# Kernel optimization log

Measured on AMD Instinct MI355X. Metric: run time of the kernel, lower is better.

Reference implementation:

```python
import jax, jax.numpy as jnp
import numpy as np

# ---- db4 filters (pywt conventions: dec_lo = rec_lo[::-1], rec_hi = qmf(rec_lo)) ----
F = 8  # db4 filter length
_rec_lo = np.array([0.23037781330885523, 0.7148465705525415, 0.6308807679295904,
                    -0.027983769416983849, -0.18703481171888114, 0.030841381835986965,
                    0.032883011666982945, -0.010597401784997278], dtype=np.float32)
_rec_hi = _rec_lo[::-1].copy()
_rec_hi[1::2] *= -1.0
REC_LO = jnp.asarray(_rec_lo)
REC_HI = jnp.asarray(_rec_hi)

MAX_LEVEL = 9  # pywt.dwt_max_level(4096, 8)


def _conv1d(x, kernel, stride=1, padding='VALID', lhs_dilation=None):
    # x: [B, L] -> correlation (XLA conv does NOT flip the kernel)
    out = jax.lax.conv_general_dilated(
        x[:, None, :], kernel[None, None, :],
        window_strides=(stride,), padding=padding,
        lhs_dilation=lhs_dilation,
        dimension_numbers=('NCH', 'OIH', 'NCH'))
    return out[:, 0, :]


def dwt(x):
    # pywt.dwt(x, 'db4', mode='symmetric'):
    # cA = np.convolve(sym_ext(x, F-1), dec_lo, 'valid')[1::2]
    # convolution with dec filter == correlation with rec filter (its reverse)
    ext = jnp.pad(x, ((0, 0), (F - 1, F - 1)), mode='symmetric')[:, 1:]
    return _conv1d(ext, REC_LO, stride=2), _conv1d(ext, REC_HI, stride=2)


def idwt(ca, cd):
    # pywt.idwt: zero-upsample coeffs, full convolution with rec filters, trim edges
    n = ca.shape[1]
    pad = ((F - 1, F - 1),)
    out = (_conv1d(ca, REC_LO[::-1], padding=pad, lhs_dilation=(2,)) +
           _conv1d(cd, REC_HI[::-1], padding=pad, lhs_dilation=(2,)))
    return out[:, F - 2:2 * n]  # output length = 2n - F + 2


def wavelet_features(x1):
    # Faithful to WaveletDWTLayer stack + WaveletParsingLayer: at each level k>=2,
    # reconstruct with details of levels k and k-1 only (others zeroed), with
    # pywt.waverec's trim-by-one rule; concatenate the 8 full-length reconstructions.
    a = x1
    cds, recs = [], []
    for level in range(1, MAX_LEVEL + 1):
        a, d = dwt(a)
        if level >= 2:
            r = idwt(jnp.zeros_like(d), d)
            for j in range(level - 2, -1, -1):
                dj = cds[j] if j == level - 2 else jnp.zeros_like(cds[j])
                if r.shape[1] == dj.shape[1] + 1:  # waverec trim rule
                    r = r[:, :-1]
                r = idwt(r, dj)
            recs.append(r)  # [B, signal_length]
        cds.append(d)
    return jnp.concatenate(recs, axis=1)  # [B, signal_length*(MAX_LEVEL-1)]


def reference(x1, x2, x3, W0, b0, W1, b1, W2, b2):
    # x2/x3 are placeholders in the original module (overwritten by layers 1/2)
    h = wavelet_features(x1)
    for W, b in ((W0, b0), (W1, b1), (W2, b2)):
        h = jax.nn.relu(h) @ W.T + b
    return h


def setup_inputs() -> dict:
    key = jax.random.key(0)
    ks = jax.random.split(key, 4)
    B, N = 2048, 4096
    D_IN, H1, H2, OUT = 32768, 181, 13, 10
    return {
        'x1': jax.random.normal(ks[0], (B, N), jnp.float32),
        'x2': jnp.zeros((B, 1, 8), jnp.float32),
        'x3': jnp.zeros((B, 1, 8), jnp.float32),
        'W0': jax.random.normal(ks[1], (H1, D_IN), jnp.float32) / np.float32(np.sqrt(D_IN)),
        'b0': jnp.zeros((H1,), jnp.float32),
        'W1': jax.random.normal(ks[2], (H2, H1), jnp.float32) / np.float32(np.sqrt(H1)),
        'b1': jnp.zeros((H2,), jnp.float32),
        'W2': jax.random.normal(ks[3], (OUT, H2), jnp.float32) / np.float32(np.sqrt(H2)),
        'b2': jnp.zeros((OUT,), jnp.float32),
    }
```

## Files before the change

kernel.cpp:

```cpp
#include <hip/hip_runtime.h>
#include <hip/hip_bf16.h>


typedef _Float16 f16x8 __attribute__((ext_vector_type(8)));
typedef _Float16 f16x4v __attribute__((ext_vector_type(4)));
typedef float f32x4 __attribute__((ext_vector_type(4)));

#define WV_THREADS 256
#define DROW 4160
#define NSPLIT 32
#define KCHUNK 1024
#define GEMM_BM 256

#define L0 0.23037781330885523f
#define L1 0.7148465705525415f
#define L2f 0.6308807679295904f
#define L3 -0.02798376941698385f
#define L4 -0.18703481171888114f
#define L5 0.030841381835986965f
#define L6 0.032883011666982945f
#define L7 -0.010597401784997278f

#define H0 -0.010597401784997278f
#define H1 -0.032883011666982945f
#define H2 0.030841381835986965f
#define H3 0.18703481171888114f
#define H4 -0.02798376941698385f
#define H5 -0.6308807679295904f
#define H6 0.7148465705525415f
#define H7 -0.23037781330885523f

__constant__ constexpr int cNL[10]   = {4096, 2051, 1029, 518, 262, 134, 70, 38, 22, 14};
__constant__ constexpr int cDOFF[10] = {0, 0, 2052, 3084, 3604, 3868, 4004, 4076, 4116, 4140};

__device__ __forceinline__ int ext_idx(int j, int n) {
  return (j < 6) ? (5 - j) : ((j < n + 6) ? (j - 6) : (2 * n + 5 - j));
}

__device__ __forceinline__ void dwt2(const float* a, float* anext, float* d,
                                     int n, int m, bool store_a) {
  const int ng = (m + 1) >> 1;
  for (int g = threadIdx.x; g < ng; g += WV_THREADS) {
    float w[10];
    if (g >= 2 && 4 * g + 9 <= n + 5) {
      const float2* af = (const float2*)a + (2 * g - 3);
      float2 b0 = af[0], b1 = af[1], b2 = af[2], b3 = af[3], b4 = af[4];
      w[0] = b0.x; w[1] = b0.y; w[2] = b1.x; w[3] = b1.y; w[4] = b2.x;
      w[5] = b2.y; w[6] = b3.x; w[7] = b3.y; w[8] = b4.x; w[9] = b4.y;
    } else {
#pragma unroll
      for (int q = 0; q < 10; ++q) {
        int j = 4 * g + q;
        int jm = n + 12;
        if (j > jm) j = jm;
        w[q] = a[ext_idx(j, n)];
      }
    }
    float sl0 = w[0]*L0 + w[1]*L1 + w[2]*L2f + w[3]*L3 + w[4]*L4 + w[5]*L5 + w[6]*L6 + w[7]*L7;
    float sh0 = w[0]*H0 + w[1]*H1 + w[2]*H2  + w[3]*H3 + w[4]*H4 + w[5]*H5 + w[6]*H6 + w[7]*H7;
    float sl1 = w[2]*L0 + w[3]*L1 + w[4]*L2f + w[5]*L3 + w[6]*L4 + w[7]*L5 + w[8]*L6 + w[9]*L7;
    float sh1 = w[2]*H0 + w[3]*H1 + w[4]*H2  + w[5]*H3 + w[6]*H4 + w[7]*H5 + w[8]*H6 + w[9]*H7;
    if (2 * g + 1 < m) {
      if (store_a) *(float2*)(anext + 2 * g) = make_float2(sl0, sl1);
      *(float2*)(d + 2 * g) = make_float2(sh0, sh1);
    } else {
      if (store_a) anext[2 * g] = sl0;
      d[2 * g] = sh0;
    }
  }
}

#define SWZ(u) ((u) ^ (((u) >> 3) & 7))
__device__ __forceinline__ const float4* lds4c(const float* b, int s) {
  return (const float4*)b + SWZ(s);
}
__device__ __forceinline__ float4* lds4(float* b, int s) {
  return (float4*)b + SWZ(s);
}

template <int NP>
__device__ __forceinline__ void lvlL(const float* a, float* v) {
#pragma unroll
  for (int q = 0; q < NP; ++q) {
    v[2*q]   = a[q+3]*L0 + a[q+2]*L2f + a[q+1]*L4 + a[q]*L6;
    v[2*q+1] = a[q+3]*L1 + a[q+2]*L3  + a[q+1]*L5 + a[q]*L7;
  }
}
template <int NP>
__device__ __forceinline__ void lvlH(const float* d, float* v) {
#pragma unroll
  for (int q = 0; q < NP; ++q) {
    v[2*q]   = d[q+3]*H0 + d[q+2]*H2 + d[q+1]*H4 + d[q]*H6;
    v[2*q+1] = d[q+3]*H1 + d[q+2]*H3 + d[q+1]*H5 + d[q]*H7;
  }
}
template <int NP>
__device__ __forceinline__ void lvlLH(const float* a, const float* d, float* v) {
#pragma unroll
  for (int q = 0; q < NP; ++q) {
    v[2*q]   = a[q+3]*L0 + a[q+2]*L2f + a[q+1]*L4 + a[q]*L6
             + d[q+3]*H0 + d[q+2]*H2  + d[q+1]*H4 + d[q]*H6;
    v[2*q+1] = a[q+3]*L1 + a[q+2]*L3  + a[q+1]*L5 + a[q]*L7
             + d[q+3]*H1 + d[q+2]*H3  + d[q+1]*H5 + d[q]*H7;
  }
}

__device__ __forceinline__ void g8f2(const float* p, int s, float* w) {
#pragma unroll
  for (int i = 0; i < 4; ++i) {
    float2 v = *(const float2*)(p + s + 2 * i);
    w[2*i] = v.x; w[2*i+1] = v.y;
  }
}
__device__ __forceinline__ void g12f4(const float* p, int s, float* w) {
#pragma unroll
  for (int i = 0; i < 3; ++i) {
    float4 v = *(const float4*)(p + s + 4 * i);
    w[4*i] = v.x; w[4*i+1] = v.y; w[4*i+2] = v.z; w[4*i+3] = v.w;
  }
}

__device__ __forceinline__ void store16(_Float16* outg, int t, const float* v) {
  f16x8 h0, h1;
#pragma unroll
  for (int i = 0; i < 8; ++i) h0[i] = (_Float16)fmaxf(v[i], 0.f);
#pragma unroll
  for (int i = 0; i < 8; ++i) h1[i] = (_Float16)fmaxf(v[8 + i], 0.f);
  *(f16x8*)(outg + 16 * t) = h0;
  *(f16x8*)(outg + 16 * t + 8) = h1;
}

__device__ __forceinline__ void fin2(const float* d2, const float* d1, _Float16* og) {
  const int t = threadIdx.x;
  float dw[12];  g12f4(d2, 4 * t, dw);
  float mid[12]; lvlH<6>(dw, mid);
  float d1w[12]; g12f4(d1, 8 * t, d1w);
  float v[16];   lvlLH<8>(mid, d1w, v);
  store16(og, t, v);
}

__device__ __forceinline__ void fin3(const float* d3, const float* d2, _Float16* og) {
  const int t = threadIdx.x;
  float dw[8];   g8f2(d3, 2 * t, dw);
  float v0[10];  lvlH<5>(dw, v0);
  float d2w[12]; g12f4(d2, 4 * t, d2w);
  float v1[12];  lvlLH<6>(v0, d2w, v1);
  float v[16];   lvlL<8>(v1, v);
  store16(og, t, v);
}

__device__ __forceinline__ void fin4(const float* d4, const float* d3, _Float16* og) {
  const int t = threadIdx.x;
  float dw[7];
#pragma unroll
  for (int i = 0; i < 7; ++i) dw[i] = d4[t + i];
  float v0[8];   lvlH<4>(dw, v0);
  float d3w[8];  g8f2(d3, 2 * t, d3w);
  float v1[10];  lvlLH<5>(v0, d3w, v1);
  float v2[12];  lvlL<6>(v1, v2);
  float v[16];   lvlL<8>(v2, v);
  store16(og, t, v);
}

template <bool HAS_CA, bool HAS_CD, bool FINAL, int N>
__device__ __forceinline__ void step16(const float* ca, const float* cd,
                                       float* outl, _Float16* outg) {
  constexpr int npair = N - 3;
  constexpr int ng = (npair + 7) >> 3;
  const int t = threadIdx.x;
  if (t >= ng) return;
  float w[12], v[12];
  if constexpr (HAS_CA) {
    float4 a = *lds4c(ca, 2 * t), b = *lds4c(ca, 2 * t + 1), c = *lds4c(ca, 2 * t + 2);
    w[0]=a.x; w[1]=a.y; w[2]=a.z; w[3]=a.w; w[4]=b.x; w[5]=b.y; w[6]=b.z; w[7]=b.w;
    w[8]=c.x; w[9]=c.y; w[10]=c.z; w[11]=c.w;
  }
  if constexpr (HAS_CD) {
    const float4* p = (const float4*)(cd + 8 * t);
    float4 a = p[0], b = p[1], c = p[2];
    v[0]=a.x; v[1]=a.y; v[2]=a.z; v[3]=a.w; v[4]=b.x; v[5]=b.y; v[6]=b.z; v[7]=b.w;
    v[8]=c.x; v[9]=c.y; v[10]=c.z; v[11]=c.w;
  }
  float E[8], O[8];
#pragma unroll
  for (int pp = 0; pp < 8; ++pp) {
    float e = 0.f, o = 0.f;
    if constexpr (HAS_CA) {
      e = w[pp+3]*L0 + w[pp+2]*L2f + w[pp+1]*L4 + w[pp]*L6;
      o = w[pp+3]*L1 + w[pp+2]*L3  + w[pp+1]*L5 + w[pp]*L7;
    }
    if constexpr (HAS_CD) {
      e += v[pp+3]*H0 + v[pp+2]*H2 + v[pp+1]*H4 + v[pp]*H6;
      o += v[pp+3]*H1 + v[pp+2]*H3 + v[pp+1]*H5 + v[pp]*H7;
    }
    E[pp] = e; O[pp] = o;
  }
  if constexpr (FINAL) {
    float vv[16];
#pragma unroll
    for (int q = 0; q < 8; ++q) { vv[2*q] = E[q]; vv[2*q+1] = O[q]; }
    store16(outg, t, vv);
  } else {
#pragma unroll
    for (int j = 0; j < 4; ++j) {
      const int p2 = 8 * t + 2 * j;
      if (p2 + 1 < npair) {
        *lds4(outl, 4 * t + j) = make_float4(E[2*j], O[2*j], E[2*j+1], O[2*j+1]);
      } else if (p2 < npair) {
        *(float2*)lds4(outl, 4 * t + j) = make_float2(E[2*j], O[2*j]);
      }
    }
  }
}

__device__ __forceinline__ void nocd2_core(const float w[12], float r[11],
                                           float E[8], float O[8]) {
#pragma unroll
  for (int h = 0; h < 6; ++h) {
    float e = w[h+3]*L0 + w[h+2]*L2f + w[h+1]*L4 + w[h]*L6;
    float o = w[h+3]*L1 + w[h+2]*L3  + w[h+1]*L5 + w[h]*L7;
    r[2*h] = e;
    if (2*h + 1 < 11) r[2*h+1] = o;
  }
#pragma unroll
  for (int pp = 0; pp < 8; ++pp) {
    E[pp] = r[pp+3]*L0 + r[pp+2]*L2f + r[pp+1]*L4 + r[pp]*L6;
    O[pp] = r[pp+3]*L1 + r[pp+2]*L3  + r[pp+1]*L5 + r[pp]*L7;
  }
}

template <int N1>
__device__ __forceinline__ void pair16(const float* cur, float* outl) {
  constexpr int N2 = (2 * N1 - 6 == 1030) ? 1029 : (2 * N1 - 6);
  constexpr int np2 = N2 - 3;
  constexpr int ng = (np2 + 7) >> 3;
  const int t = threadIdx.x;
  if (t >= ng) return;
  float w[12];
  float4 a = *lds4c(cur, t), b = *lds4c(cur, t + 1), c = *lds4c(cur, t + 2);
  w[0]=a.x; w[1]=a.y; w[2]=a.z; w[3]=a.w; w[4]=b.x; w[5]=b.y; w[6]=b.z; w[7]=b.w;
  w[8]=c.x; w[9]=c.y; w[10]=c.z; w[11]=c.w;
  float r[11], E[8], O[8];
  nocd2_core(w, r, E, O);
#pragma unroll
  for (int j = 0; j < 4; ++j) {
    const int p2 = 8 * t + 2 * j;
    if (p2 + 1 < np2) {
      *lds4(outl, 4 * t + j) = make_float4(E[2*j], O[2*j], E[2*j+1], O[2*j+1]);
    } else if (p2 < np2) {
      *(float2*)lds4(outl, 4 * t + j) = make_float2(E[2*j], O[2*j]);
    }
  }
}

__device__ __forceinline__ void finpair16(const float* cur, _Float16* outg) {
  const int t = threadIdx.x;
  float w[12];
  float4 a = *lds4c(cur, t), b = *lds4c(cur, t + 1), c = *lds4c(cur, t + 2);
  w[0]=a.x; w[1]=a.y; w[2]=a.z; w[3]=a.w; w[4]=b.x; w[5]=b.y; w[6]=b.z; w[7]=b.w;
  w[8]=c.x; w[9]=c.y; w[10]=c.z; w[11]=c.w;
  float r[11], E[8], O[8];
  nocd2_core(w, r, E, O);
  float vv[16];
#pragma unroll
  for (int q = 0; q < 8; ++q) { vv[2*q] = E[q]; vv[2*q+1] = O[q]; }
  store16(outg, t, vv);
}

template <int NL, int NLm1>
__device__ __forceinline__ void initpair16(const float* cdL, const float* cdm,
                                           float* outl) {
  constexpr int np2 = NLm1 - 3;
  constexpr int ng = (np2 + 7) >> 3;
  const int t = threadIdx.x;
  if (t >= ng) return;
  float w[12];
  {
    const float4* p = (const float4*)(cdL + 4 * t);
    float4 a = p[0], b = p[1], c = p[2];
    w[0]=a.x; w[1]=a.y; w[2]=a.z; w[3]=a.w; w[4]=b.x; w[5]=b.y; w[6]=b.z; w[7]=b.w;
    w[8]=c.x; w[9]=c.y; w[10]=c.z; w[11]=c.w;
  }
  float r[11];
#pragma unroll
  for (int h = 0; h < 6; ++h) {
    float e = w[h+3]*H0 + w[h+2]*H2 + w[h+1]*H4 + w[h]*H6;
    float o = w[h+3]*H1 + w[h+2]*H3 + w[h+1]*H5 + w[h]*H7;
    r[2*h] = e;
    if (2*h + 1 < 11) r[2*h+1] = o;
  }
  float v[12];
  {
    const float4* p = (const float4*)(cdm + 8 * t);
    float4 a = p[0], b = p[1], c = p[2];
    v[0]=a.x; v[1]=a.y; v[2]=a.z; v[3]=a.w; v[4]=b.x; v[5]=b.y; v[6]=b.z; v[7]=b.w;
    v[8]=c.x; v[9]=c.y; v[10]=c.z; v[11]=c.w;
  }
  float E[8], O[8];
#pragma unroll
  for (int pp = 0; pp < 8; ++pp) {
    E[pp] = r[pp+3]*L0 + r[pp+2]*L2f + r[pp+1]*L4 + r[pp]*L6
          + v[pp+3]*H0 + v[pp+2]*H2  + v[pp+1]*H4 + v[pp]*H6;
    O[pp] = r[pp+3]*L1 + r[pp+2]*L3  + r[pp+1]*L5 + r[pp]*L7
          + v[pp+3]*H1 + v[pp+2]*H3  + v[pp+1]*H5 + v[pp]*H7;
  }
#pragma unroll
  for (int j = 0; j < 4; ++j) {
    const int p2 = 8 * t + 2 * j;
    if (p2 + 1 < np2) {
      *lds4(outl, 4 * t + j) = make_float4(E[2*j], O[2*j], E[2*j+1], O[2*j+1]);
    } else if (p2 < np2) {
      *(float2*)lds4(outl, 4 * t + j) = make_float2(E[2*j], O[2*j]);
    }
  }
}

__global__ __launch_bounds__(WV_THREADS) void wv_analysis_cvt(
    const float* __restrict__ x, float* __restrict__ dG,
    const float* __restrict__ W0, _Float16* __restrict__ Bw) {
  __shared__ float r1[4104];
  __shared__ float r2[2056];
  const int tid = threadIdx.x;

  if (blockIdx.x >= 2048) {
    size_t i = ((size_t)(blockIdx.x - 2048) * 256 + tid) * 4;
    int rowc = (int)(i >> 15);
    f16x4v h;
    if (rowc < 181) {
      const float4 v = *(const float4*)(W0 + i);
      h[0] = (_Float16)v.x; h[1] = (_Float16)v.y;
      h[2] = (_Float16)v.z; h[3] = (_Float16)v.w;
    } else {
      h[0] = (_Float16)0.f; h[1] = (_Float16)0.f;
      h[2] = (_Float16)0.f; h[3] = (_Float16)0.f;
    }
    *(f16x4v*)(Bw + i) = h;
    return;
  }

  const int NLa[10]  = {4096, 2051, 1029, 518, 262, 134, 70, 38, 22, 14};
  const int DOFF[10] = {0, 0, 2052, 3084, 3604, 3868, 4004, 4076, 4116, 4140};
  const int LOFF[10] = {0, 0, 1036, 520, 2068, 1040, 2332, 1176, 2404, 1216};
  const int row = blockIdx.x;

  const float4* xr = (const float4*)(x + (size_t)row * 4096);
  for (int i = tid; i < 1024; i += WV_THREADS) ((float4*)r1)[i] = xr[i];
  __syncthreads();

  float* dr = dG + (size_t)row * DROW;
  dwt2(r1, r2, dr + DOFF[1], NLa[0], NLa[1], true);
  __syncthreads();
  const float* ap = r2;
  float* an = r1;
  for (int lev = 2; lev <= 9; ++lev) {
    float* dbuf = ((lev & 1) ? r2 : r1) + LOFF[lev];
    dwt2(ap, an, dbuf, NLa[lev - 1], NLa[lev], lev < 9);
    __syncthreads();
    const float* t = ap; ap = an; an = (float*)t;
  }
  for (int lev = 2; lev <= 9; ++lev) {
    const float* src = ((lev & 1) ? r2 : r1) + LOFF[lev];
    float* dst = dr + DOFF[lev];
    const int n = NLa[lev];
    for (int i = 2 * tid; i + 1 < n; i += 2 * WV_THREADS)
      *(float2*)(dst + i) = *(const float2*)(src + i);
    if ((n & 1) && tid == 0) dst[n - 1] = src[n - 1];
  }
}

__global__ __launch_bounds__(WV_THREADS, 8) void wv_synth(
    const float* __restrict__ dG, _Float16* __restrict__ A) {
  __shared__ alignas(16) float s1[2080];
  __shared__ alignas(16) float s2[2080];
  const int row = blockIdx.x;
  const float* dr = dG + (size_t)row * DROW;
  _Float16* og = A + (size_t)row * 32768 + (size_t)blockIdx.y * 4096;
  switch (blockIdx.y) {
    case 0: fin2(dr + cDOFF[2], dr + cDOFF[1], og); break;
    case 1: fin3(dr + cDOFF[3], dr + cDOFF[2], og); break;
    case 2: fin4(dr + cDOFF[4], dr + cDOFF[3], og); break;
    case 3:
      initpair16<cNL[5], cNL[4]>(dr + cDOFF[5], dr + cDOFF[4], s1);
      __syncthreads();
      pair16<518>(s1, s2); __syncthreads();
      step16<true, false, true, 2051>(s2, nullptr, nullptr, og);
      break;
    case 4:
      initpair16<cNL[6], cNL[5]>(dr + cDOFF[6], dr + cDOFF[5], s1);
      __syncthreads();
      pair16<262>(s1, s2); __syncthreads();
      finpair16(s2, og);
      break;
    case 5:
      initpair16<cNL[7], cNL[6]>(dr + cDOFF[7], dr + cDOFF[6], s1);
      __syncthreads();
      pair16<134>(s1, s2); __syncthreads();
      pair16<518>(s2, s1); __syncthreads();
      step16<true, false, true, 2051>(s1, nullptr, nullptr, og);
      break;
    case 6:
      initpair16<cNL[8], cNL[7]>(dr + cDOFF[8], dr + cDOFF[7], s1);
      __syncthreads();
      pair16<70>(s1, s2); __syncthreads();
      pair16<262>(s2, s1); __syncthreads();
      finpair16(s1, og);
      break;
    default:
      initpair16<cNL[9], cNL[8]>(dr + cDOFF[9], dr + cDOFF[8], s1);
      __syncthreads();
      pair16<38>(s1, s2); __syncthreads();
      pair16<134>(s2, s1); __syncthreads();
      pair16<518>(s1, s2); __syncthreads();
      step16<true, false, true, 2051>(s2, nullptr, nullptr, og);
      break;
  }
}

__device__ __forceinline__ void load_lds16(const void* g, void* l) {
  __builtin_amdgcn_global_load_lds((__attribute__((address_space(1))) unsigned int*)g,
                                   (__attribute__((address_space(3))) unsigned int*)l,
                                   16, 0, 0);
}

__global__ __launch_bounds__(512, 2) void gemm_kernel(
    const _Float16* __restrict__ A, const _Float16* __restrict__ Bw,
    float* __restrict__ P) {
  __shared__ _Float16 As[2][GEMM_BM * 64];
  __shared__ _Float16 Bs[2][192 * 64];
  const int tid = threadIdx.x;
  const int lane = tid & 63;
  const int wave = tid >> 6;
  const int m0 = blockIdx.x * GEMM_BM;
  const int k_idx = blockIdx.y;
  const int k0 = k_idx * KCHUNK;

  f32x4 acc[2][12];
#pragma unroll
  for (int mt = 0; mt < 2; ++mt)
#pragma unroll
    for (int nt = 0; nt < 12; ++nt) acc[mt][nt] = (f32x4){0.f, 0.f, 0.f, 0.f};

  auto stage = [&](int ks, int b) {
    const int kbase = k0 + (ks << 6);
#pragma unroll
    for (int t = 0; t < 4; ++t) {
      int c = wave * 4 + t;
      int g = (c << 6) + lane;
      int r = g >> 3, cs = g & 7;
      const _Float16* gp = A + (size_t)(m0 + r) * 32768 + kbase + ((cs ^ (r & 7)) << 3);
      load_lds16(gp, (char*)As[b] + ((size_t)c << 10));
    }
#pragma unroll
    for (int t = 0; t < 3; ++t) {
      int c = wave * 3 + t;
      int g = (c << 6) + lane;
      int r = g >> 3, cs = g & 7;
      const _Float16* gp = Bw + (size_t)r * 32768 + kbase + ((cs ^ (r & 7)) << 3);
      load_lds16(gp, (char*)Bs[b] + ((size_t)c << 10));
    }
  };

  auto compute = [&](int cur) {
#pragma unroll
    for (int kk = 0; kk < 2; ++kk) {
      const int chunk = kk * 4 + (lane >> 4);
      f16x8 af[2];
#pragma unroll
      for (int mt = 0; mt < 2; ++mt) {
        int r = wave * 32 + mt * 16 + (lane & 15);
        af[mt] = *(const f16x8*)(As[cur] + r * 64 + ((chunk ^ (r & 7)) << 3));
      }
#pragma unroll
      for (int nt = 0; nt < 12; ++nt) {
        int rb = nt * 16 + (lane & 15);
        f16x8 bf = *(const f16x8*)(Bs[cur] + rb * 64 + ((chunk ^ (rb & 7)) << 3));
        acc[0][nt] = __builtin_amdgcn_mfma_f32_16x16x32_f16(af[0], bf, acc[0][nt], 0, 0, 0);
        acc[1][nt] = __builtin_amdgcn_mfma_f32_16x16x32_f16(af[1], bf, acc[1][nt], 0, 0, 0);
      }
    }
  };

  constexpr int NT = KCHUNK >> 6;
  stage(0, 0);
  for (int ks = 0; ks < NT - 1; ++ks) {
    stage(ks + 1, (ks + 1) & 1);
    asm volatile("s_waitcnt vmcnt(7)" ::: "memory");
    __builtin_amdgcn_s_barrier();
    compute(ks & 1);
    __builtin_amdgcn_s_barrier();
  }
  asm volatile("s_waitcnt vmcnt(0)" ::: "memory");
  __builtin_amdgcn_s_barrier();
  compute((NT - 1) & 1);

  float* Pp = P + ((size_t)k_idx * 2048 + m0) * 192;
#pragma unroll
  for (int mt = 0; mt < 2; ++mt)
#pragma unroll
    for (int nt = 0; nt < 12; ++nt)
#pragma unroll
      for (int r4 = 0; r4 < 4; ++r4) {
        int rr = wave * 32 + mt * 16 + ((lane >> 4) << 2) + r4;
        int cc = nt * 16 + (lane & 15);
        Pp[(size_t)rr * 192 + cc] = acc[mt][nt][r4];
      }
}

__global__ __launch_bounds__(256) void mlp_kernel(
    const float* __restrict__ P, const float* __restrict__ b0,
    const float* __restrict__ W1, const float* __restrict__ b1,
    const float* __restrict__ W2, const float* __restrict__ b2,
    float* __restrict__ out) {
  __shared__ float part[4][193];
  __shared__ float h1[192];
  __shared__ float h2[13];
  const int row = blockIdx.x;
  const int t = threadIdx.x;
  const int g = t >> 6;
  const int l = t & 63;

  float a0 = 0.f, a1 = 0.f, a2 = 0.f;
  for (int si = 0; si < NSPLIT / 4; ++si) {
    int s = g + (si << 2);
    const float* Pr = P + ((size_t)s * 2048 + row) * 192;
    a0 += Pr[l]; a1 += Pr[64 + l]; a2 += Pr[128 + l];
  }
  part[g][l] = a0; part[g][64 + l] = a1; part[g][128 + l] = a2;
  __syncthreads();

  if (t < 192) {
    float v = part[0][t] + part[1][t] + part[2][t] + part[3][t];
    h1[t] = (t < 181) ? fmaxf(v + b0[t], 0.f) : 0.f;
  }
  __syncthreads();

#pragma unroll
  for (int r = 0; r < 4; ++r) {
    int j = g + (r << 2);
    if (j < 13) {
      float v = 0.f;
#pragma unroll
      for (int q = 0; q < 3; ++q) {
        int n = l + (q << 6);
        if (n < 181) v += h1[n] * W1[j * 181 + n];
      }
      for (int off = 32; off >= 1; off >>= 1) v += __shfl_down(v, off);
      if (l == 0) h2[j] = fmaxf(v + b1[j], 0.f);
    }
  }
  __syncthreads();

  if (t < 10) {
    float c = b2[t];
#pragma unroll
    for (int j = 0; j < 13; ++j) c += h2[j] * W2[t * 13 + j];
    out[(size_t)row * 10 + t] = c;
  }
}

extern "C" void kernel_launch(void* const* d_in, const int* in_sizes, int n_in,
                              void* d_out, int out_size, void* d_ws, size_t ws_size,
                              hipStream_t stream) {
  const float* x1 = (const float*)d_in[0];
  const float* W0 = (const float*)d_in[3];
  const float* b0 = (const float*)d_in[4];
  const float* W1 = (const float*)d_in[5];
  const float* b1 = (const float*)d_in[6];
  const float* W2 = (const float*)d_in[7];
  const float* b2 = (const float*)d_in[8];
  float* out = (float*)d_out;

  char* ws = (char*)d_ws;
  const size_t A_BYTES = (size_t)2048 * 32768 * 2;
  const size_t B_BYTES = (size_t)192 * 32768 * 2;
  _Float16* Afeat = (_Float16*)ws;
  _Float16* Bw = (_Float16*)(ws + A_BYTES);
  float* Dq = (float*)(ws + A_BYTES + B_BYTES);
  float* P = (float*)(ws + A_BYTES + B_BYTES);

  wv_analysis_cvt<<<2048 + 6144, WV_THREADS, 0, stream>>>(x1, Dq, W0, Bw);
  dim3 sg(2048, 8);
  wv_synth<<<sg, WV_THREADS, 0, stream>>>(Dq, Afeat);
  dim3 gg(2048 / GEMM_BM, NSPLIT);
  gemm_kernel<<<gg, 512, 0, stream>>>(Afeat, Bw, P);
  mlp_kernel<<<2048, 256, 0, stream>>>(P, b0, W1, b1, W2, b2, out);
}
```

Before: 222.1 us.

## Fuse wavelet analysis and synthesis into one per-row kernel using LDS

Merges the analysis kernel and the 8-way synthesis kernel into a single per-row kernel. Detail coefficients now stay in shared memory instead of being written to and reread from a global scratch buffer, and one launch is removed. The synthesis of all 8 levels now runs serially inside one block per row rather than across 8 blocks per row. That cuts parallelism and raises LDS use per block (occupancy hint 3), which is the risk. The single-step helper is also simplified to the low-pass-only path.

Measured after the change: 236.4 us. 1.06x slower.

```diff
diff --git a/kernel.cpp b/kernel.cpp
--- a/kernel.cpp
+++ b/kernel.cpp
@@ -7,7 +7,6 @@
 typedef float f32x4 __attribute__((ext_vector_type(4)));
 
 #define WV_THREADS 256
-#define DROW 4160
 #define NSPLIT 32
 #define KCHUNK 1024
 #define GEMM_BM 256
@@ -30,8 +29,7 @@
 #define H6 0.7148465705525415f
 #define H7 -0.23037781330885523f
 
-__constant__ constexpr int cNL[10]   = {4096, 2051, 1029, 518, 262, 134, 70, 38, 22, 14};
-__constant__ constexpr int cDOFF[10] = {0, 0, 2052, 3084, 3604, 3868, 4004, 4076, 4116, 4140};
+__constant__ constexpr int cNL[10] = {4096, 2051, 1029, 518, 262, 134, 70, 38, 22, 14};
 
 __device__ __forceinline__ int ext_idx(int j, int n) {
   return (j < 6) ? (5 - j) : ((j < n + 6) ? (j - 6) : (2 * n + 5 - j));
@@ -162,52 +160,27 @@
   store16(og, t, v);
 }
 
-template <bool HAS_CA, bool HAS_CD, bool FINAL, int N>
-__device__ __forceinline__ void step16(const float* ca, const float* cd,
-                                       float* outl, _Float16* outg) {
+template <bool FINAL, int N>
+__device__ __forceinline__ void stepL(const float* ca, float* outl, _Float16* outg) {
   constexpr int npair = N - 3;
   constexpr int ng = (npair + 7) >> 3;
   const int t = threadIdx.x;
   if (t >= ng) return;
-  float w[12], v[12];
-  if constexpr (HAS_CA) {
-    float4 a = *lds4c(ca, 2 * t), b = *lds4c(ca, 2 * t + 1), c = *lds4c(ca, 2 * t + 2);
-    w[0]=a.x; w[1]=a.y; w[2]=a.z; w[3]=a.w; w[4]=b.x; w[5]=b.y; w[6]=b.z; w[7]=b.w;
-    w[8]=c.x; w[9]=c.y; w[10]=c.z; w[11]=c.w;
-  }
-  if constexpr (HAS_CD) {
-    const float4* p = (const float4*)(cd + 8 * t);
-    float4 a = p[0], b = p[1], c = p[2];
-    v[0]=a.x; v[1]=a.y; v[2]=a.z; v[3]=a.w; v[4]=b.x; v[5]=b.y; v[6]=b.z; v[7]=b.w;
-    v[8]=c.x; v[9]=c.y; v[10]=c.z; v[11]=c.w;
-  }
-  float E[8], O[8];
-#pragma unroll
-  for (int pp = 0; pp < 8; ++pp) {
-    float e = 0.f, o = 0.f;
-    if constexpr (HAS_CA) {
-      e = w[pp+3]*L0 + w[pp+2]*L2f + w[pp+1]*L4 + w[pp]*L6;
-      o = w[pp+3]*L1 + w[pp+2]*L3  + w[pp+1]*L5 + w[pp]*L7;
-    }
-    if constexpr (HAS_CD) {
-      e += v[pp+3]*H0 + v[pp+2]*H2 + v[pp+1]*H4 + v[pp]*H6;
-      o += v[pp+3]*H1 + v[pp+2]*H3 + v[pp+1]*H5 + v[pp]*H7;
-    }
-    E[pp] = e; O[pp] = o;
-  }
+  float w[12];
+  float4 a = *lds4c(ca, 2 * t), b = *lds4c(ca, 2 * t + 1), c = *lds4c(ca, 2 * t + 2);
+  w[0]=a.x; w[1]=a.y; w[2]=a.z; w[3]=a.w; w[4]=b.x; w[5]=b.y; w[6]=b.z; w[7]=b.w;
+  w[8]=c.x; w[9]=c.y; w[10]=c.z; w[11]=c.w;
+  float v[16]; lvlL<8>(w, v);
   if constexpr (FINAL) {
-    float vv[16];
-#pragma unroll
-    for (int q = 0; q < 8; ++q) { vv[2*q] = E[q]; vv[2*q+1] = O[q]; }
-    store16(outg, t, vv);
+    store16(outg, t, v);
   } else {
 #pragma unroll
     for (int j = 0; j < 4; ++j) {
       const int p2 = 8 * t + 2 * j;
       if (p2 + 1 < npair) {
-        *lds4(outl, 4 * t + j) = make_float4(E[2*j], O[2*j], E[2*j+1], O[2*j+1]);
+        *lds4(outl, 4 * t + j) = make_float4(v[4*j], v[4*j+1], v[4*j+2], v[4*j+3]);
       } else if (p2 < npair) {
-        *(float2*)lds4(outl, 4 * t + j) = make_float2(E[2*j], O[2*j]);
+        *(float2*)lds4(outl, 4 * t + j) = make_float2(v[4*j], v[4*j+1]);
       }
     }
   }
@@ -274,13 +247,7 @@
   constexpr int ng = (np2 + 7) >> 3;
   const int t = threadIdx.x;
   if (t >= ng) return;
-  float w[12];
-  {
-    const float4* p = (const float4*)(cdL + 4 * t);
-    float4 a = p[0], b = p[1], c = p[2];
-    w[0]=a.x; w[1]=a.y; w[2]=a.z; w[3]=a.w; w[4]=b.x; w[5]=b.y; w[6]=b.z; w[7]=b.w;
-    w[8]=c.x; w[9]=c.y; w[10]=c.z; w[11]=c.w;
-  }
+  float w[12]; g12f4(cdL, 4 * t, w);
   float r[11];
 #pragma unroll
   for (int h = 0; h < 6; ++h) {
@@ -289,13 +256,7 @@
     r[2*h] = e;
     if (2*h + 1 < 11) r[2*h+1] = o;
   }
-  float v[12];
-  {
-    const float4* p = (const float4*)(cdm + 8 * t);
-    float4 a = p[0], b = p[1], c = p[2];
-    v[0]=a.x; v[1]=a.y; v[2]=a.z; v[3]=a.w; v[4]=b.x; v[5]=b.y; v[6]=b.z; v[7]=b.w;
-    v[8]=c.x; v[9]=c.y; v[10]=c.z; v[11]=c.w;
-  }
+  float v[12]; g12f4(cdm, 8 * t, v);
   float E[8], O[8];
 #pragma unroll
   for (int pp = 0; pp < 8; ++pp) {
@@ -315,11 +276,14 @@
   }
 }
 
-__global__ __launch_bounds__(WV_THREADS) void wv_analysis_cvt(
-    const float* __restrict__ x, float* __restrict__ dG,
+__global__ __launch_bounds__(WV_THREADS, 3) void wv_row_cvt(
+    const float* __restrict__ x, _Float16* __restrict__ A,
     const float* __restrict__ W0, _Float16* __restrict__ Bw) {
-  __shared__ float r1[4104];
-  __shared__ float r2[2056];
+  __shared__ alignas(16) float r1[4104];
+  __shared__ alignas(16) float r2[2056];
+  __shared__ alignas(16) float d1b[2052];
+  __shared__ alignas(16) float s1[2080];
+  __shared__ alignas(16) float s2[2080];
   const int tid = threadIdx.x;
 
   if (blockIdx.x >= 2048) {
@@ -339,7 +303,6 @@
   }
 
   const int NLa[10]  = {4096, 2051, 1029, 518, 262, 134, 70, 38, 22, 14};
-  const int DOFF[10] = {0, 0, 2052, 3084, 3604, 3868, 4004, 4076, 4116, 4140};
   const int LOFF[10] = {0, 0, 1036, 520, 2068, 1040, 2332, 1176, 2404, 1216};
   const int row = blockIdx.x;
 
@@ -347,8 +310,7 @@
   for (int i = tid; i < 1024; i += WV_THREADS) ((float4*)r1)[i] = xr[i];
   __syncthreads();
 
-  float* dr = dG + (size_t)row * DROW;
-  dwt2(r1, r2, dr + DOFF[1], NLa[0], NLa[1], true);
+  dwt2(r1, r2, d1b, NLa[0], NLa[1], true);
   __syncthreads();
   const float* ap = r2;
   float* an = r1;
@@ -358,62 +320,41 @@
     __syncthreads();
     const float* t = ap; ap = an; an = (float*)t;
   }
-  for (int lev = 2; lev <= 9; ++lev) {
-    const float* src = ((lev & 1) ? r2 : r1) + LOFF[lev];
-    float* dst = dr + DOFF[lev];
-    const int n = NLa[lev];
-    for (int i = 2 * tid; i + 1 < n; i += 2 * WV_THREADS)
-      *(float2*)(dst + i) = *(const float2*)(src + i);
-    if ((n & 1) && tid == 0) dst[n - 1] = src[n - 1];
-  }
-}
-
-__global__ __launch_bounds__(WV_THREADS, 8) void wv_synth(
-    const float* __restrict__ dG, _Float16* __restrict__ A) {
-  __shared__ alignas(16) float s1[2080];
-  __shared__ alignas(16) float s2[2080];
-  const int row = blockIdx.x;
-  const float* dr = dG + (size_t)row * DROW;
-  _Float16* og = A + (size_t)row * 32768 + (size_t)blockIdx.y * 4096;
-  switch (blockIdx.y) {
-    case 0: fin2(dr + cDOFF[2], dr + cDOFF[1], og); break;
-    case 1: fin3(dr + cDOFF[3], dr + cDOFF[2], og); break;
-    case 2: fin4(dr + cDOFF[4], dr + cDOFF[3], og); break;
-    case 3:
-      initpair16<cNL[5], cNL[4]>(dr + cDOFF[5], dr + cDOFF[4], s1);
-      __syncthreads();
-      pair16<518>(s1, s2); __syncthreads();
-      step16<true, false, true, 2051>(s2, nullptr, nullptr, og);
-      break;
-    case 4:
-      initpair16<cNL[6], cNL[5]>(dr + cDOFF[6], dr + cDOFF[5], s1);
-      __syncthreads();
-      pair16<262>(s1, s2); __syncthreads();
-      finpair16(s2, og);
-      break;
-    case 5:
-      initpair16<cNL[7], cNL[6]>(dr + cDOFF[7], dr + cDOFF[6], s1);
-      __syncthreads();
-      pair16<134>(s1, s2); __syncthreads();
-      pair16<518>(s2, s1); __syncthreads();
-      step16<true, false, true, 2051>(s1, nullptr, nullptr, og);
-      break;
-    case 6:
-      initpair16<cNL[8], cNL[7]>(dr + cDOFF[8], dr + cDOFF[7], s1);
-      __syncthreads();
-      pair16<70>(s1, s2); __syncthreads();
-      pair16<262>(s2, s1); __syncthreads();
-      finpair16(s1, og);
-      break;
-    default:
-      initpair16<cNL[9], cNL[8]>(dr + cDOFF[9], dr + cDOFF[8], s1);
-      __syncthreads();
-      pair16<38>(s1, s2); __syncthreads();
-      pair16<134>(s2, s1); __syncthreads();
-      pair16<518>(s1, s2); __syncthreads();
-      step16<true, false, true, 2051>(s2, nullptr, nullptr, og);
-      break;
-  }
+  const float* d2 = r1 + 1036;  const float* d3 = r2 + 520;
+  const float* d4 = r1 + 2068;  const float* d5 = r2 + 1040;
+  const float* d6 = r1 + 2332;  const float* d7 = r2 + 1176;
+  const float* d8 = r1 + 2404;  const float* d9 = r2 + 1216;
+
+  _Float16* og = A + (size_t)row * 32768;
+
+  fin2(d2, d1b, og);
+  fin3(d3, d2, og + 4096);
+  fin4(d4, d3, og + 8192);
+
+  initpair16<cNL[5], cNL[4]>(d5, d4, s1);
+  __syncthreads();
+  pair16<518>(s1, s2); __syncthreads();
+  stepL<true, 2051>(s2, nullptr, og + 3 * 4096);
+  initpair16<cNL[6], cNL[5]>(d6, d5, s1);
+  __syncthreads();
+  pair16<262>(s1, s2); __syncthreads();
+  finpair16(s2, og + 4 * 4096);
+  initpair16<cNL[7], cNL[6]>(d7, d6, s1);
+  __syncthreads();
+  pair16<134>(s1, s2); __syncthreads();
+  pair16<518>(s2, s1); __syncthreads();
+  stepL<true, 2051>(s1, nullptr, og + 5 * 4096);
+  initpair16<cNL[8], cNL[7]>(d8, d7, s1);
+  __syncthreads();
+  pair16<70>(s1, s2); __syncthreads();
+  pair16<262>(s2, s1); __syncthreads();
+  finpair16(s1, og + 6 * 4096);
+  initpair16<cNL[9], cNL[8]>(d9, d8, s1);
+  __syncthreads();
+  pair16<38>(s1, s2); __syncthreads();
+  pair16<134>(s2, s1); __syncthreads();
+  pair16<518>(s1, s2); __syncthreads();
+  stepL<true, 2051>(s2, nullptr, og + 7 * 4096);
 }
 
 __device__ __forceinline__ void load_lds16(const void* g, void* l) {
@@ -575,12 +516,9 @@
   const size_t B_BYTES = (size_t)192 * 32768 * 2;
   _Float16* Afeat = (_Float16*)ws;
   _Float16* Bw = (_Float16*)(ws + A_BYTES);
-  float* Dq = (float*)(ws + A_BYTES + B_BYTES);
   float* P = (float*)(ws + A_BYTES + B_BYTES);
 
-  wv_analysis_cvt<<<2048 + 6144, WV_THREADS, 0, stream>>>(x1, Dq, W0, Bw);
-  dim3 sg(2048, 8);
-  wv_synth<<<sg, WV_THREADS, 0, stream>>>(Dq, Afeat);
+  wv_row_cvt<<<2048 + 6144, WV_THREADS, 0, stream>>>(x1, Afeat, W0, Bw);
   dim3 gg(2048 / GEMM_BM, NSPLIT);
   gemm_kernel<<<gg, 512, 0, stream>>>(Afeat, Bw, P);
   mlp_kernel<<<2048, 256, 0, stream>>>(P, b0, W1, b1, W2, b2, out);
```
